# Optimization experiments

Measured on AMD Instinct MI355X. Metric: run time of the kernel, lower is better.

## Reference

```python
import jax, jax.numpy as jnp
import numpy as np

B, S, D, H, DK, DV = 4, 1024, 1024, 16, 64, 64
NEG = jnp.float32(-1e10)


def setup_inputs() -> dict:
    key = jax.random.key(0)
    ks = jax.random.split(key, 9)
    q = jax.random.normal(ks[0], (B, S, D), dtype=jnp.float32)
    k = jax.random.normal(ks[1], (B, S, D), dtype=jnp.float32)
    v = jax.random.normal(ks[2], (B, S, D), dtype=jnp.float32)
    pad_mask_1 = jax.random.randint(ks[3], (B,), 1, S + 1, dtype=jnp.int32)
    pad_mask_2 = jax.random.randint(ks[4], (B,), 1, S + 1, dtype=jnp.int32)
    # Per-head projection weights stacked over heads (torch Linear, bias=False).
    sc = 1.0 / np.sqrt(D)
    Wq = jax.random.uniform(ks[5], (H, D, DK), jnp.float32, -sc, sc)
    Wk = jax.random.uniform(ks[6], (H, D, DK), jnp.float32, -sc, sc)
    Wv = jax.random.uniform(ks[7], (H, D, DV), jnp.float32, -sc, sc)
    Wo = jax.random.uniform(ks[8], (H * DV, D), jnp.float32, -sc, sc)
    return {"q": q, "k": k, "v": v, "pad_mask_1": pad_mask_1,
            "pad_mask_2": pad_mask_2, "Wq": Wq, "Wk": Wk, "Wv": Wv, "Wo": Wo}


def reference(q, k, v, pad_mask_1, pad_mask_2, Wq, Wk, Wv, Wo):
    Bq, Sq, _ = q.shape
    scale = jnp.sqrt(jnp.float32(Wq.shape[-1]))
    qh = jnp.einsum('bsd,hdk->bhsk', q, Wq)   # [B,H,S,DK]
    kh = jnp.einsum('bsd,hdk->bhsk', k, Wk)
    vh = jnp.einsum('bsd,hdv->bhsv', v, Wv)
    w = jnp.einsum('bhqk,bhtk->bhqt', qh, kh) / scale  # [B,H,S,S]
    idx = jnp.arange(Sq)
    # pad_mask_1: mask key columns >= length; pad_mask_2: mask query rows >= length
    key_dead = idx[None, :] >= pad_mask_1[:, None]      # [B,S]
    row_dead = idx[None, :] >= pad_mask_2[:, None]      # [B,S]
    w = jnp.where(key_dead[:, None, None, :], NEG, w)
    w = jnp.where(row_dead[:, None, :, None], NEG, w)
    # causal: w.tril() + (-1e10).triu(1) == keep lower triangle, NEG strictly above
    causal = idx[None, :] > idx[:, None]                # [S,S] strictly upper
    w = jnp.where(causal[None, None], NEG, w)
    a = jax.nn.softmax(w, axis=-1)
    o = jnp.einsum('bhqt,bhtv->bhqv', a, vh)            # [B,H,S,DV]
    o = o.transpose(0, 2, 1, 3).reshape(Bq, Sq, -1)     # concat heads (head-major)
    return o @ Wo
```

## Files before the change

kernel.cpp:

```cpp
#include <hip/hip_runtime.h>

#define B_ 4
#define S_ 1024
#define D_ 1024
#define H_ 16
#define BSD (B_*S_*D_)

typedef unsigned short ushort_t;
typedef __attribute__((ext_vector_type(8))) __bf16 bf16x8;
typedef __attribute__((ext_vector_type(8))) ushort_t ushortx8;
typedef __attribute__((ext_vector_type(4))) float f32x4;

__device__ __forceinline__ ushort_t f2bf(float f) {
  union { float f; unsigned int u; } x; x.f = f;
  unsigned int r = x.u + 0x7fffu + ((x.u >> 16) & 1u);
  return (ushort_t)(r >> 16);
}

__device__ __forceinline__ void gll16(const void* g, void* l) {
  __builtin_amdgcn_global_load_lds(
      (const __attribute__((address_space(1))) unsigned int*)g,
      (__attribute__((address_space(3))) unsigned int*)l, 16, 0, 0);
}

__global__ __launch_bounds__(256) void transpose_w(
    const float* __restrict__ Wq, const float* __restrict__ Wk,
    const float* __restrict__ Wv, const float* __restrict__ Wo,
    ushort_t* __restrict__ WqT, ushort_t* __restrict__ WkT,
    ushort_t* __restrict__ WvT, ushort_t* __restrict__ WoT)
{
  __shared__ float tile[64][65];
  int blk = blockIdx.x;
  const float* src; ushort_t* dst;
  size_t sbase, dbase; int ld_src, ld_dst, r0, c0;
  if (blk < 768) {
    int tz = blk / 256;
    int rem = blk % 256; int head = rem >> 4; int kt = rem & 15;
    src = (tz == 0) ? Wq : (tz == 1) ? Wk : Wv;
    dst = (tz == 0) ? WqT : (tz == 1) ? WkT : WvT;
    sbase = (size_t)head * 1024 * 64; dbase = (size_t)head * 64 * 1024;
    ld_src = 64; ld_dst = 1024; r0 = kt * 64; c0 = 0;
  } else {
    int idx = blk - 768; src = Wo; dst = WoT;
    sbase = 0; dbase = 0; ld_src = 1024; ld_dst = 1024;
    r0 = (idx >> 4) * 64; c0 = (idx & 15) * 64;
  }
  int tid = threadIdx.x; int col = tid & 63; int rbase = tid >> 6;
  #pragma unroll
  for (int j = 0; j < 16; ++j) {
    int row = j * 4 + rbase;
    tile[row][col] = src[sbase + (size_t)(r0 + row) * ld_src + c0 + col];
  }
  __syncthreads();
  #pragma unroll
  for (int j = 0; j < 16; ++j) {
    int orow = j * 4 + rbase;
    dst[dbase + (size_t)(c0 + orow) * ld_dst + r0 + col] = f2bf(tile[col][orow]);
  }
}

__device__ __forceinline__ void gemm_body_f32A(
    const float* __restrict__ Af, const ushort_t* __restrict__ BT,
    ushort_t* __restrict__ Cb, int epi, int m0, int n0, int K)
{
  __shared__ __align__(16) ushort_t As[2][128 * 64];
  __shared__ __align__(16) ushort_t Bs[2][128 * 64];
  const int tid = threadIdx.x;
  const int wave = tid >> 6, lane = tid & 63;
  const int wm = wave >> 2, wn = wave & 3;

  f32x4 acc[4][2] = {};
  float4 aA[2][2], aB[2][2];

  auto loadA = [&](float4 (&dst)[2][2], int k0) {
    #pragma unroll
    for (int i = 0; i < 2; ++i) {
      int off = ((i * 8 + wave) << 10) + lane * 16;
      int row = off >> 7;
      int cb = off & 127;
      int lcb = cb ^ ((row & 7) << 4);
      const float* src = Af + (size_t)(m0 + row) * K + k0 + (lcb >> 1);
      dst[i][0] = *(const float4*)(src);
      dst[i][1] = *(const float4*)(src + 4);
    }
  };
  auto writeA = [&](int buf, const float4 (&src)[2][2]) {
    #pragma unroll
    for (int i = 0; i < 2; ++i) {
      int off = ((i * 8 + wave) << 10) + lane * 16;
      ushortx8 tv;
      #pragma unroll
      for (int j = 0; j < 4; ++j) {
        tv[j]     = f2bf(((const float*)&src[i][0])[j]);
        tv[4 + j] = f2bf(((const float*)&src[i][1])[j]);
      }
      *(ushortx8*)((char*)As[buf] + off) = tv;
    }
  };
  auto stageB = [&](int buf, int k0) {
    #pragma unroll
    for (int i = 0; i < 2; ++i) {
      int off = ((i * 8 + wave) << 10) + lane * 16;
      int row = off >> 7;
      int cb = off & 127;
      int lcb = cb ^ ((row & 7) << 4);
      gll16(BT + (size_t)(n0 + row) * K + k0 + (lcb >> 1), (char*)Bs[buf] + off);
    }
  };

  auto compute = [&](int buf) {
    #pragma unroll
    for (int kk = 0; kk < 2; ++kk) {
      bf16x8 af[4], bfr[2];
      #pragma unroll
      for (int mf = 0; mf < 4; ++mf) {
        int row = wm * 64 + mf * 16 + (lane & 15);
        int cb = kk * 64 + ((lane >> 4) << 4);
        af[mf] = *(const bf16x8*)((const char*)As[buf] + (row << 7) + (cb ^ ((row & 7) << 4)));
      }
      #pragma unroll
      for (int nf = 0; nf < 2; ++nf) {
        int row = wn * 32 + nf * 16 + (lane & 15);
        int cb = kk * 64 + ((lane >> 4) << 4);
        bfr[nf] = *(const bf16x8*)((const char*)Bs[buf] + (row << 7) + (cb ^ ((row & 7) << 4)));
      }
      #pragma unroll
      for (int mf = 0; mf < 4; ++mf)
        #pragma unroll
        for (int nf = 0; nf < 2; ++nf)
          acc[mf][nf] = __builtin_amdgcn_mfma_f32_16x16x32_bf16(af[mf], bfr[nf], acc[mf][nf], 0, 0, 0);
    }
  };

#define CBAR4() do { asm volatile("s_waitcnt vmcnt(4) lgkmcnt(0)" ::: "memory"); \
                     __builtin_amdgcn_s_barrier(); } while (0)

  const int nt = K >> 6;
  loadA(aA, 0);
  stageB(0, 0);
  writeA(0, aA);
  loadA(aA, 64);
  CBAR4();

  for (int t = 0; t < nt - 2; t += 2) {
    stageB(1, (t + 1) << 6);
    loadA(aB, (t + 2) << 6);
    __builtin_amdgcn_sched_barrier(0);
    compute(0);
    writeA(1, aA);
    CBAR4();
    stageB(0, (t + 2) << 6);
    loadA(aA, (t + 3) << 6);
    __builtin_amdgcn_sched_barrier(0);
    compute(1);
    writeA(0, aB);
    CBAR4();
  }
  stageB(1, (nt - 1) << 6);
  __builtin_amdgcn_sched_barrier(0);
  compute(0);
  writeA(1, aA);
  asm volatile("s_waitcnt vmcnt(0) lgkmcnt(0)" ::: "memory");
  __builtin_amdgcn_s_barrier();
  compute(1);

#undef CBAR4

  #pragma unroll
  for (int mf = 0; mf < 4; ++mf) {
    #pragma unroll
    for (int nf = 0; nf < 2; ++nf) {
      #pragma unroll
      for (int r = 0; r < 4; ++r) {
        int m = m0 + wm * 64 + mf * 16 + ((lane >> 4) << 2) + r;
        int n = n0 + wn * 32 + nf * 16 + (lane & 15);
        float val = acc[mf][nf][r];
        if (epi == 0) {
          int b = m >> 10, s = m & 1023, h = n >> 6, dk = n & 63;
          Cb[((((size_t)(b * H_ + h)) << 10) + s) * 64 + dk] = f2bf(val);
        } else {
          int b = m >> 10, s = m & 1023, h = n >> 6, dv = n & 63;
          Cb[((((size_t)(b * H_ + h)) * 64 + dv) << 10) + s] = f2bf(val);
        }
      }
    }
  }
}

__device__ __forceinline__ void gemm_body(
    const ushort_t* __restrict__ A, const ushort_t* __restrict__ BT,
    float* __restrict__ Cf, int m0, int n0, int K)
{
  __shared__ __align__(16) ushort_t As[2][128 * 64];
  __shared__ __align__(16) ushort_t Bs[2][128 * 64];
  const int tid = threadIdx.x;
  const int wave = tid >> 6, lane = tid & 63;
  const int wm = wave >> 2, wn = wave & 3;

  f32x4 acc[4][2] = {};

  auto stage = [&](int buf, int k0) {
    #pragma unroll
    for (int i = 0; i < 2; ++i) {
      int off = ((i * 8 + wave) << 10) + lane * 16;
      int row = off >> 7;
      int cb = off & 127;
      int lcb = cb ^ ((row & 7) << 4);
      gll16(A + (size_t)(m0 + row) * K + k0 + (lcb >> 1), (char*)As[buf] + off);
      gll16(BT + (size_t)(n0 + row) * K + k0 + (lcb >> 1), (char*)Bs[buf] + off);
    }
  };

  auto compute = [&](int buf) {
    #pragma unroll
    for (int kk = 0; kk < 2; ++kk) {
      bf16x8 af[4], bfr[2];
      #pragma unroll
      for (int mf = 0; mf < 4; ++mf) {
        int row = wm * 64 + mf * 16 + (lane & 15);
        int cb = kk * 64 + ((lane >> 4) << 4);
        af[mf] = *(const bf16x8*)((const char*)As[buf] + (row << 7) + (cb ^ ((row & 7) << 4)));
      }
      #pragma unroll
      for (int nf = 0; nf < 2; ++nf) {
        int row = wn * 32 + nf * 16 + (lane & 15);
        int cb = kk * 64 + ((lane >> 4) << 4);
        bfr[nf] = *(const bf16x8*)((const char*)Bs[buf] + (row << 7) + (cb ^ ((row & 7) << 4)));
      }
      #pragma unroll
      for (int mf = 0; mf < 4; ++mf)
        #pragma unroll
        for (int nf = 0; nf < 2; ++nf)
          acc[mf][nf] = __builtin_amdgcn_mfma_f32_16x16x32_bf16(af[mf], bfr[nf], acc[mf][nf], 0, 0, 0);
    }
  };

  const int nt = K >> 6;
  stage(0, 0);
  __syncthreads();
  int cur = 0;
  for (int t = 0; t < nt - 1; ++t) {
    stage(cur ^ 1, (t + 1) << 6);
    compute(cur);
    __syncthreads();
    cur ^= 1;
  }
  compute(cur);

  #pragma unroll
  for (int mf = 0; mf < 4; ++mf) {
    #pragma unroll
    for (int nf = 0; nf < 2; ++nf) {
      #pragma unroll
      for (int r = 0; r < 4; ++r) {
        int m = m0 + wm * 64 + mf * 16 + ((lane >> 4) << 2) + r;
        int n = n0 + wn * 32 + nf * 16 + (lane & 15);
        Cf[(size_t)m * 1024 + n] = acc[mf][nf][r];
      }
    }
  }
}

__global__ __launch_bounds__(512, 4) void proj_gemm(
    const float* q, const float* k, const float* v,
    const ushort_t* WqT, const ushort_t* WkT, const ushort_t* WvT,
    ushort_t* qh, ushort_t* kh, ushort_t* vhT)
{
  int f = blockIdx.x;
  int xcd = f & 7;
  int slot = f >> 3;
  int g = xcd * 12 + (slot >> 3);
  int y = slot & 7;
  int z = g >> 5, x = g & 31;
  const float* A = (z == 0) ? q : (z == 1) ? k : v;
  const ushort_t* BT = (z == 0) ? WqT : (z == 1) ? WkT : WvT;
  ushort_t* C = (z == 0) ? qh : (z == 1) ? kh : vhT;
  gemm_body_f32A(A, BT, C, (z == 2) ? 1 : 0, x * 128, y * 128, 1024);
}

__global__ __launch_bounds__(512, 4) void out_gemm(
    const ushort_t* o, const ushort_t* WoT, float* out)
{
  int f = blockIdx.x;
  int xcd = f & 7;
  int slot = f >> 3;
  int x = xcd * 4 + (slot >> 3);
  int y = slot & 7;
  gemm_body(o, WoT, out, x * 128, y * 128, 1024);
}

__global__ __launch_bounds__(256) void meanv_kernel(
    const ushort_t* __restrict__ vhT, float* __restrict__ meanV)
{
  int row = blockIdx.x * 4 + (threadIdx.x >> 6);
  int lane = threadIdx.x & 63;
  const ushort_t* src = vhT + ((size_t)row << 10) + lane * 16;
  float s = 0.f;
  #pragma unroll
  for (int i = 0; i < 2; ++i) {
    bf16x8 v = *(const bf16x8*)(src + i * 8);
    #pragma unroll
    for (int j = 0; j < 8; ++j) s += (float)v[j];
  }
  #pragma unroll
  for (int mm = 1; mm < 64; mm <<= 1) s += __shfl_xor(s, mm);
  if (lane == 0) meanV[row] = s * (1.0f / 1024.0f);
}

__global__ __launch_bounds__(256) void attn_kernel(
    const ushort_t* __restrict__ qh, const ushort_t* __restrict__ kh,
    const ushort_t* __restrict__ vhT, const float* __restrict__ meanV,
    const int* __restrict__ pad1p, const int* __restrict__ pad2p,
    ushort_t* __restrict__ o)
{
  const int bh = blockIdx.x;
  const int b = bh >> 4, h = bh & 15;
  const int q0 = blockIdx.y << 6;
  const int pad1 = pad1p[b], pad2 = pad2p[b];
  const int tid = threadIdx.x, wave = tid >> 6, lane = tid & 63;

  if (q0 >= pad2) {
    int dv = tid & 63;
    int rw = tid >> 6;
    ushort_t mb = f2bf(meanV[(bh << 6) + dv]);
    for (int r = rw; r < 64; r += 4)
      o[(((size_t)((b << 10) + q0 + r)) << 10) + (h << 6) + dv] = mb;
    return;
  }

  __shared__ __align__(16) ushort_t Ks[64 * 64];
  __shared__ __align__(16) ushort_t Vs[64 * 64];
  __shared__ __align__(16) ushort_t Ps[4][16 * 64];

  const ushort_t* qbase = qh + ((size_t)bh << 16);
  const ushort_t* kbase = kh + ((size_t)bh << 16);
  const ushort_t* vbase = vhT + ((size_t)bh << 16);

  const int qrow = q0 + wave * 16 + (lane & 15);
  bf16x8 qf[2];
  qf[0] = *(const bf16x8*)(qbase + (size_t)qrow * 64 + ((lane >> 4) << 3));
  qf[1] = *(const bf16x8*)(qbase + (size_t)qrow * 64 + 32 + ((lane >> 4) << 3));

  f32x4 acc[4] = {};
  float mrow[4] = { -1e30f, -1e30f, -1e30f, -1e30f };
  float lrow[4] = { 0.f, 0.f, 0.f, 0.f };
  const int ribase = q0 + wave * 16 + ((lane >> 4) << 2);

  int t_hi = min(q0 + 63, min(pad2 - 1, pad1 - 1));
  int nb = (t_hi >> 6) + 1;

  for (int kb = 0; kb < nb; ++kb) {
    const int t0 = kb << 6;
    #pragma unroll
    for (int i = 0; i < 2; ++i) {
      int off = ((i * 4 + wave) << 10) + lane * 16;
      int row = off >> 7;
      int cb = off & 127;
      int lcb = cb ^ ((row & 7) << 4);
      gll16(kbase + (size_t)(t0 + row) * 64 + (lcb >> 1), (char*)Ks + off);
      gll16(vbase + ((size_t)row << 10) + t0 + (lcb >> 1), (char*)Vs + off);
    }
    __syncthreads();

    f32x4 sc[4];
    #pragma unroll
    for (int nf = 0; nf < 4; ++nf) {
      sc[nf] = (f32x4){0.f, 0.f, 0.f, 0.f};
      #pragma unroll
      for (int kk = 0; kk < 2; ++kk) {
        int trow = nf * 16 + (lane & 15);
        int cb = kk * 64 + ((lane >> 4) << 4);
        bf16x8 kf = *(const bf16x8*)((const char*)Ks + (trow << 7) + (cb ^ ((trow & 7) << 4)));
        sc[nf] = __builtin_amdgcn_mfma_f32_16x16x32_bf16(qf[kk], kf, sc[nf], 0, 0, 0);
      }
    }

    float pv[4][4];
    #pragma unroll
    for (int r = 0; r < 4; ++r) {
      const int irow = ribase + r;
      float sval[4];
      float rmax = -1e30f;
      #pragma unroll
      for (int nf = 0; nf < 4; ++nf) {
        int t = t0 + nf * 16 + (lane & 15);
        float vv = sc[nf][r] * 0.125f;
        if (t > irow || t >= pad1) vv = -1e10f;
        sval[nf] = vv;
        rmax = fmaxf(rmax, vv);
      }
      #pragma unroll
      for (int mm = 1; mm < 16; mm <<= 1) rmax = fmaxf(rmax, __shfl_xor(rmax, mm));
      float nm = fmaxf(mrow[r], rmax);
      float fscale = __expf(mrow[r] - nm);
      float rsum = 0.f;
      #pragma unroll
      for (int nf = 0; nf < 4; ++nf) {
        float p = __expf(sval[nf] - nm);
        pv[nf][r] = p;
        rsum += p;
      }
      #pragma unroll
      for (int mm = 1; mm < 16; mm <<= 1) rsum += __shfl_xor(rsum, mm);
      mrow[r] = nm;
      lrow[r] = lrow[r] * fscale + rsum;
      #pragma unroll
      for (int dvf = 0; dvf < 4; ++dvf) acc[dvf][r] *= fscale;
    }

    #pragma unroll
    for (int nf = 0; nf < 4; ++nf) {
      #pragma unroll
      for (int r = 0; r < 4; ++r) {
        int prow = ((lane >> 4) << 2) + r;
        int cbw = (nf * 16 + (lane & 15)) * 2;
        *(ushort_t*)((char*)Ps[wave] + (prow << 7) + (cbw ^ ((prow & 7) << 4))) = f2bf(pv[nf][r]);
      }
    }

    #pragma unroll
    for (int kk = 0; kk < 2; ++kk) {
      int prow = lane & 15;
      int cb = kk * 64 + ((lane >> 4) << 4);
      bf16x8 pf = *(const bf16x8*)((const char*)Ps[wave] + (prow << 7) + (cb ^ ((prow & 7) << 4)));
      #pragma unroll
      for (int dvf = 0; dvf < 4; ++dvf) {
        int vrow = dvf * 16 + (lane & 15);
        bf16x8 vfr = *(const bf16x8*)((const char*)Vs + (vrow << 7) + (cb ^ ((vrow & 7) << 4)));
        acc[dvf] = __builtin_amdgcn_mfma_f32_16x16x32_bf16(pf, vfr, acc[dvf], 0, 0, 0);
      }
    }
    __syncthreads();
  }

  #pragma unroll
  for (int dvf = 0; dvf < 4; ++dvf) {
    #pragma unroll
    for (int r = 0; r < 4; ++r) {
      int irow = ribase + r;
      int dv = dvf * 16 + (lane & 15);
      float val;
      if (irow < pad2) val = acc[dvf][r] * (1.0f / lrow[r]);
      else val = meanV[(bh << 6) + dv];
      o[(((size_t)((b << 10) + irow)) << 10) + (h << 6) + dv] = f2bf(val);
    }
  }
}

extern "C" void kernel_launch(void* const* d_in, const int* in_sizes, int n_in,
                              void* d_out, int out_size, void* d_ws, size_t ws_size,
                              hipStream_t stream) {
  (void)in_sizes; (void)n_in; (void)out_size; (void)ws_size;
  const float* q = (const float*)d_in[0];
  const float* k = (const float*)d_in[1];
  const float* v = (const float*)d_in[2];
  const int* pad1 = (const int*)d_in[3];
  const int* pad2 = (const int*)d_in[4];
  const float* Wq = (const float*)d_in[5];
  const float* Wk = (const float*)d_in[6];
  const float* Wv = (const float*)d_in[7];
  const float* Wo = (const float*)d_in[8];
  float* out = (float*)d_out;

  char* ws = (char*)d_ws;
  const size_t MB = 1u << 20;
  ushort_t* WqT = (ushort_t*)(ws + 24 * MB);
  ushort_t* WkT = (ushort_t*)(ws + 26 * MB);
  ushort_t* WvT = (ushort_t*)(ws + 28 * MB);
  ushort_t* WoT = (ushort_t*)(ws + 30 * MB);
  ushort_t* qh  = (ushort_t*)(ws + 32 * MB);
  ushort_t* kh  = (ushort_t*)(ws + 40 * MB);
  ushort_t* vhT = (ushort_t*)(ws + 48 * MB);
  ushort_t* ob  = (ushort_t*)(ws + 56 * MB);
  float* meanV  = (float*)(ws + 64 * MB);

  transpose_w<<<1024, 256, 0, stream>>>(Wq, Wk, Wv, Wo, WqT, WkT, WvT, WoT);
  proj_gemm<<<768, 512, 0, stream>>>(q, k, v, WqT, WkT, WvT, qh, kh, vhT);
  meanv_kernel<<<1024, 256, 0, stream>>>(vhT, meanV);
  attn_kernel<<<dim3(64, 16), 256, 0, stream>>>(qh, kh, vhT, meanV, pad1, pad2, ob);
  out_gemm<<<256, 512, 0, stream>>>(ob, WoT, out);
}
```

Before: 108.7 us.

## Replace direct-to-LDS loads with register-staged double-buffered pipeline in both GEMMs

Both projection and output GEMMs drop global_load_lds for the B operand (and for A in the bf16 GEMM). They now load A and B into registers one tile ahead, write them to LDS after the compute step, and sync with an lgkmcnt-only barrier. Address offsets are precomputed once outside the loop. The aim is to hide global latency behind MFMA work and make the two GEMMs share one schedule, at the cost of more VGPRs and extra LDS write instructions.

```diff
diff --git a/kernel.cpp b/kernel.cpp
--- a/kernel.cpp
+++ b/kernel.cpp
@@ -22,6 +22,10 @@
       (const __attribute__((address_space(1))) unsigned int*)g,
       (__attribute__((address_space(3))) unsigned int*)l, 16, 0, 0);
 }
+
+#define PBAR() do { asm volatile("s_waitcnt lgkmcnt(0)" ::: "memory"); \
+                    __builtin_amdgcn_s_barrier(); \
+                    asm volatile("" ::: "memory"); } while (0)
 
 __global__ __launch_bounds__(256) void transpose_w(
     const float* __restrict__ Wq, const float* __restrict__ Wk,
@@ -59,7 +63,7 @@
   }
 }
 
-__device__ __forceinline__ void gemm_body_f32A(
+__device__ __forceinline__ void gemm_pipe_f32A(
     const float* __restrict__ Af, const ushort_t* __restrict__ BT,
     ushort_t* __restrict__ Cb, int epi, int m0, int n0, int K)
 {
@@ -70,44 +74,41 @@
   const int wm = wave >> 2, wn = wave & 3;
 
   f32x4 acc[4][2] = {};
-  float4 aA[2][2], aB[2][2];
-
-  auto loadA = [&](float4 (&dst)[2][2], int k0) {
+  float4   ra0[2][2], ra1[2][2];
+  ushortx8 rb0[2],    rb1[2];
+
+  int offs[2], gofs[2];
+  #pragma unroll
+  for (int i = 0; i < 2; ++i) {
+    int off = ((i * 8 + wave) << 10) + lane * 16;
+    int row = off >> 7, cb = off & 127;
+    int lcb = cb ^ ((row & 7) << 4);
+    offs[i] = off;
+    gofs[i] = row * K + (lcb >> 1);
+  }
+
+  auto loadAB = [&](float4 (&ar)[2][2], ushortx8 (&br)[2], int k0) {
     #pragma unroll
     for (int i = 0; i < 2; ++i) {
-      int off = ((i * 8 + wave) << 10) + lane * 16;
-      int row = off >> 7;
-      int cb = off & 127;
-      int lcb = cb ^ ((row & 7) << 4);
-      const float* src = Af + (size_t)(m0 + row) * K + k0 + (lcb >> 1);
-      dst[i][0] = *(const float4*)(src);
-      dst[i][1] = *(const float4*)(src + 4);
-    }
-  };
-  auto writeA = [&](int buf, const float4 (&src)[2][2]) {
+      const float* asrc = Af + (size_t)m0 * K + gofs[i] + k0;
+      ar[i][0] = *(const float4*)(asrc);
+      ar[i][1] = *(const float4*)(asrc + 4);
+      br[i] = *(const ushortx8*)(BT + (size_t)n0 * K + gofs[i] + k0);
+    }
+  };
+  auto writeAB = [&](int buf, const float4 (&ar)[2][2], const ushortx8 (&br)[2]) {
     #pragma unroll
     for (int i = 0; i < 2; ++i) {
-      int off = ((i * 8 + wave) << 10) + lane * 16;
       ushortx8 tv;
       #pragma unroll
       for (int j = 0; j < 4; ++j) {
-        tv[j]     = f2bf(((const float*)&src[i][0])[j]);
-        tv[4 + j] = f2bf(((const float*)&src[i][1])[j]);
-      }
-      *(ushortx8*)((char*)As[buf] + off) = tv;
-    }
-  };
-  auto stageB = [&](int buf, int k0) {
-    #pragma unroll
-    for (int i = 0; i < 2; ++i) {
-      int off = ((i * 8 + wave) << 10) + lane * 16;
-      int row = off >> 7;
-      int cb = off & 127;
-      int lcb = cb ^ ((row & 7) << 4);
-      gll16(BT + (size_t)(n0 + row) * K + k0 + (lcb >> 1), (char*)Bs[buf] + off);
-    }
-  };
-
+        tv[j]     = f2bf(((const float*)&ar[i][0])[j]);
+        tv[4 + j] = f2bf(((const float*)&ar[i][1])[j]);
+      }
+      *(ushortx8*)((char*)As[buf] + offs[i]) = tv;
+      *(ushortx8*)((char*)Bs[buf] + offs[i]) = br[i];
+    }
+  };
   auto compute = [&](int buf) {
     #pragma unroll
     for (int kk = 0; kk < 2; ++kk) {
@@ -132,39 +133,28 @@
     }
   };
 
-#define CBAR4() do { asm volatile("s_waitcnt vmcnt(4) lgkmcnt(0)" ::: "memory"); \
-                     __builtin_amdgcn_s_barrier(); } while (0)
-
   const int nt = K >> 6;
-  loadA(aA, 0);
-  stageB(0, 0);
-  writeA(0, aA);
-  loadA(aA, 64);
-  CBAR4();
-
-  for (int t = 0; t < nt - 2; t += 2) {
-    stageB(1, (t + 1) << 6);
-    loadA(aB, (t + 2) << 6);
+  loadAB(ra0, rb0, 0);
+  writeAB(0, ra0, rb0);
+  loadAB(ra1, rb1, 64);
+  PBAR();
+
+  for (int t = 0; t < nt - 3; t += 2) {
+    loadAB(ra0, rb0, (t + 2) << 6);
     __builtin_amdgcn_sched_barrier(0);
     compute(0);
-    writeA(1, aA);
-    CBAR4();
-    stageB(0, (t + 2) << 6);
-    loadA(aA, (t + 3) << 6);
+    writeAB(1, ra1, rb1);
+    PBAR();
+    loadAB(ra1, rb1, (t + 3) << 6);
     __builtin_amdgcn_sched_barrier(0);
     compute(1);
-    writeA(0, aB);
-    CBAR4();
-  }
-  stageB(1, (nt - 1) << 6);
-  __builtin_amdgcn_sched_barrier(0);
+    writeAB(0, ra0, rb0);
+    PBAR();
+  }
   compute(0);
-  writeA(1, aA);
-  asm volatile("s_waitcnt vmcnt(0) lgkmcnt(0)" ::: "memory");
-  __builtin_amdgcn_s_barrier();
+  writeAB(1, ra1, rb1);
+  PBAR();
   compute(1);
-
-#undef CBAR4
 
   #pragma unroll
   for (int mf = 0; mf < 4; ++mf) {
@@ -187,7 +177,7 @@
   }
 }
 
-__device__ __forceinline__ void gemm_body(
+__device__ __forceinline__ void gemm_pipe_bf16(
     const ushort_t* __restrict__ A, const ushort_t* __restrict__ BT,
     float* __restrict__ Cf, int m0, int n0, int K)
 {
@@ -198,19 +188,32 @@
   const int wm = wave >> 2, wn = wave & 3;
 
   f32x4 acc[4][2] = {};
-
-  auto stage = [&](int buf, int k0) {
+  ushortx8 ra0[2], ra1[2], rb0[2], rb1[2];
+
+  int offs[2], gofs[2];
+  #pragma unroll
+  for (int i = 0; i < 2; ++i) {
+    int off = ((i * 8 + wave) << 10) + lane * 16;
+    int row = off >> 7, cb = off & 127;
+    int lcb = cb ^ ((row & 7) << 4);
+    offs[i] = off;
+    gofs[i] = row * K + (lcb >> 1);
+  }
+
+  auto loadAB = [&](ushortx8 (&ar)[2], ushortx8 (&br)[2], int k0) {
     #pragma unroll
     for (int i = 0; i < 2; ++i) {
-      int off = ((i * 8 + wave) << 10) + lane * 16;
-      int row = off >> 7;
-      int cb = off & 127;
-      int lcb = cb ^ ((row & 7) << 4);
-      gll16(A + (size_t)(m0 + row) * K + k0 + (lcb >> 1), (char*)As[buf] + off);
-      gll16(BT + (size_t)(n0 + row) * K + k0 + (lcb >> 1), (char*)Bs[buf] + off);
-    }
-  };
-
+      ar[i] = *(const ushortx8*)(A  + (size_t)m0 * K + gofs[i] + k0);
+      br[i] = *(const ushortx8*)(BT + (size_t)n0 * K + gofs[i] + k0);
+    }
+  };
+  auto writeAB = [&](int buf, const ushortx8 (&ar)[2], const ushortx8 (&br)[2]) {
+    #pragma unroll
+    for (int i = 0; i < 2; ++i) {
+      *(ushortx8*)((char*)As[buf] + offs[i]) = ar[i];
+      *(ushortx8*)((char*)Bs[buf] + offs[i]) = br[i];
+    }
+  };
   auto compute = [&](int buf) {
     #pragma unroll
     for (int kk = 0; kk < 2; ++kk) {
@@ -236,16 +239,27 @@
   };
 
   const int nt = K >> 6;
-  stage(0, 0);
-  __syncthreads();
-  int cur = 0;
-  for (int t = 0; t < nt - 1; ++t) {
-    stage(cur ^ 1, (t + 1) << 6);
-    compute(cur);
-    __syncthreads();
-    cur ^= 1;
-  }
-  compute(cur);
+  loadAB(ra0, rb0, 0);
+  writeAB(0, ra0, rb0);
+  loadAB(ra1, rb1, 64);
+  PBAR();
+
+  for (int t = 0; t < nt - 3; t += 2) {
+    loadAB(ra0, rb0, (t + 2) << 6);
+    __builtin_amdgcn_sched_barrier(0);
+    compute(0);
+    writeAB(1, ra1, rb1);
+    PBAR();
+    loadAB(ra1, rb1, (t + 3) << 6);
+    __builtin_amdgcn_sched_barrier(0);
+    compute(1);
+    writeAB(0, ra0, rb0);
+    PBAR();
+  }
+  compute(0);
+  writeAB(1, ra1, rb1);
+  PBAR();
+  compute(1);
 
   #pragma unroll
   for (int mf = 0; mf < 4; ++mf) {
@@ -275,7 +289,7 @@
   const float* A = (z == 0) ? q : (z == 1) ? k : v;
   const ushort_t* BT = (z == 0) ? WqT : (z == 1) ? WkT : WvT;
   ushort_t* C = (z == 0) ? qh : (z == 1) ? kh : vhT;
-  gemm_body_f32A(A, BT, C, (z == 2) ? 1 : 0, x * 128, y * 128, 1024);
+  gemm_pipe_f32A(A, BT, C, (z == 2) ? 1 : 0, x * 128, y * 128, 1024);
 }
 
 __global__ __launch_bounds__(512, 4) void out_gemm(
@@ -286,7 +300,7 @@
   int slot = f >> 3;
   int x = xcd * 4 + (slot >> 3);
   int y = slot & 7;
-  gemm_body(o, WoT, out, x * 128, y * 128, 1024);
+  gemm_pipe_bf16(o, WoT, out, x * 128, y * 128, 1024);
 }
 
 __global__ __launch_bounds__(256) void meanv_kernel(
```

Result: faster. 99.02 us (-8.9%).
